# Kernel optimization log

Hardware: AMD Instinct MI355X
Metric: run time of the kernel (lower is better)

## Reference

```python
import jax, jax.numpy as jnp
import numpy as np

B, C, H, W = 16, 256, 32, 32
LN_EPS = 1e-5


def setup_inputs() -> dict:
    key = jax.random.key(0)
    ks = jax.random.split(key, 12)
    s = 1.0 / np.sqrt(C)
    x = jax.random.normal(ks[0], (B, C, H, W), dtype=jnp.float32)
    # Linear weights stored as [in, out] (torch stores [out, in]; math is x @ W_in_out + b)
    wq = jax.random.uniform(ks[1], (C, C), jnp.float32, -s, s)
    bq = jax.random.uniform(ks[2], (C,), jnp.float32, -s, s)
    wk = jax.random.uniform(ks[3], (C, C), jnp.float32, -s, s)
    bk = jax.random.uniform(ks[4], (C,), jnp.float32, -s, s)
    wv = jax.random.uniform(ks[5], (C, C), jnp.float32, -s, s)
    bv = jax.random.uniform(ks[6], (C,), jnp.float32, -s, s)
    w1 = jax.random.uniform(ks[7], (C, C), jnp.float32, -s, s)
    b1 = jax.random.uniform(ks[8], (C,), jnp.float32, -s, s)
    w2 = jax.random.uniform(ks[9], (C, C), jnp.float32, -s, s)
    b2 = jax.random.uniform(ks[10], (C,), jnp.float32, -s, s)
    gamma = jnp.ones((C,), jnp.float32)
    beta = jnp.zeros((C,), jnp.float32)
    return {"x": x, "wq": wq, "bq": bq, "wk": wk, "bk": bk, "wv": wv, "bv": bv,
            "w1": w1, "b1": b1, "w2": w2, "b2": b2, "gamma": gamma, "beta": beta}


def reference(x, wq, bq, wk, bk, wv, bv, w1, b1, w2, b2, gamma, beta):
    Bd, Cd, Hd, Wd = x.shape
    t = x.reshape(Bd, Cd, Hd * Wd).transpose(0, 2, 1)  # [B, N, C]
    q = t @ wq + bq
    k = t @ wk + bk
    v = t @ wv + bv
    # matrix[b,i,j] = q[b,i,:] . k[b,j,:]  (no 1/sqrt(d) scaling, as in source)
    m = jnp.einsum('bic,bjc->bij', q, k)
    # softmax over dim=-2 (the query axis i)
    m = jax.nn.softmax(m, axis=-2)
    # att[b,j,c] = sum_i v[b,i,c] * m[b,i,j]  (v^T @ m, then permute)
    att = jnp.einsum('bic,bij->bjc', v, m)  # [B, N, C]
    # MLP (SiLU, hidden = C), dropout p=0 -> identity; DropPath eval -> identity
    att = jax.nn.silu(att @ w1 + b1) @ w2 + b2
    # LayerNorm over channel dim
    mu = jnp.mean(att, axis=-1, keepdims=True)
    var = jnp.var(att, axis=-1, keepdims=True)
    att = (att - mu) * jax.lax.rsqrt(var + LN_EPS) * gamma + beta
    return att.transpose(0, 2, 1).reshape(Bd, Cd, Hd, Wd)
```

## Files before the change

### kernel.cpp

```cpp
#include <hip/hip_runtime.h>

#define BB 16
#define CC 256
#define NN 1024

typedef _Float16 f16;
typedef __attribute__((ext_vector_type(8))) _Float16 half8;
typedef __attribute__((ext_vector_type(4))) float f32x4;

__device__ __forceinline__ half8 ldg8(const f16* p) {
  return *reinterpret_cast<const half8*>(p);
}

__device__ __forceinline__ void gll16(const f16* g, f16* l) {
  __builtin_amdgcn_global_load_lds((const __attribute__((address_space(1))) void*)g,
                                   (__attribute__((address_space(3))) void*)l, 16, 0, 0);
}

#define VMCNT(n) asm volatile("s_waitcnt vmcnt(" #n ")" ::: "memory")
#define BAR() __builtin_amdgcn_s_barrier()

__device__ __forceinline__ void stage64k(const f16* __restrict__ g, f16* l, int wave, int lane) {
#pragma unroll
  for (int k = 0; k < 16; ++k) {
    int ob = k * 2048 + wave * 512;
    gll16(g + ob + lane * 8, l + ob);
  }
}

struct WP5 {
  const float* s[5];
  f16* d[5];
};

__global__ void __launch_bounds__(256) k_packW(WP5 p) {
  __shared__ float ws[256][17];
  int m = blockIdx.y, ct = blockIdx.x;
  const float* W = p.s[m];
  f16* wp = p.d[m];
  int tid = threadIdx.x;
  int col = tid & 15, cig = tid >> 4;
#pragma unroll
  for (int pg = 0; pg < 16; ++pg) {
    int ci = pg * 16 + cig;
    ws[ci][col] = W[(size_t)ci * 256 + ct * 16 + col];
  }
  __syncthreads();
  int lane = tid & 63, wave = tid >> 6;
  int row16 = lane & 15, quad = lane >> 4;
#pragma unroll
  for (int kk = 0; kk < 2; ++kk) {
    int kc = wave * 2 + kk;
    half8 o;
#pragma unroll
    for (int j = 0; j < 8; ++j) o[j] = (f16)ws[kc * 32 + quad * 8 + j][row16];
    *reinterpret_cast<half8*>(wp + ((size_t)ct * 8 + kc) * 512 + lane * 8) = o;
  }
}

struct QkvSmem {
  union {
    struct { f16 hi[32][264]; f16 lo[32][264]; } ts;
    f16 ex[2][16][264];
    f16 exv[256][40];
  };
};

__global__ void __launch_bounds__(256) k_qkv(const float* __restrict__ x,
    const f16* __restrict__ wqp, const f16* __restrict__ wkp, const f16* __restrict__ wvp,
    const float* __restrict__ bq, const float* __restrict__ bk, const float* __restrict__ bv,
    f16* __restrict__ qp, f16* __restrict__ kp, f16* __restrict__ vp, int b_base) {
  __shared__ QkvSmem sm;
  int bl = blockIdx.x, bg = b_base + bl, n0 = blockIdx.y * 32;
  int tid = threadIdx.x, wave = tid >> 6, lane = tid & 63;
  int row16 = lane & 15, quad = lane >> 4;
  int g = wave >> 1, h = wave & 1;

#pragma unroll
  for (int e = tid; e < 2048; e += 256) {
    int c = e >> 3, n4 = (e & 7) << 2;
    float4 u = *reinterpret_cast<const float4*>(x + (size_t)(bg * CC + c) * NN + n0 + n4);
    float uv[4] = {u.x, u.y, u.z, u.w};
#pragma unroll
    for (int i = 0; i < 4; ++i) {
      f16 hh = (f16)uv[i];
      sm.ts.hi[n4 + i][c] = hh;
      sm.ts.lo[n4 + i][c] = (f16)(uv[i] - (float)hh);
    }
  }
  __syncthreads();

  half8 ah[8], al[8];
#pragma unroll
  for (int kc = 0; kc < 8; ++kc) {
    ah[kc] = *reinterpret_cast<const half8*>(&sm.ts.hi[g * 16 + row16][kc * 32 + quad * 8]);
    al[kc] = *reinterpret_cast<const half8*>(&sm.ts.lo[g * 16 + row16][kc * 32 + quad * 8]);
  }
  __syncthreads();

  const f16* WTs[2]    = {wqp, wkp};
  const float* biases[2] = {bq, bk};
  f16* outs[2]         = {qp, kp};
#pragma unroll
  for (int z = 0; z < 2; ++z) {
    const f16* WT = WTs[z];
    const float* bias = biases[z];
    f16* outp = outs[z];
#pragma unroll
    for (int cp = 0; cp < 2; ++cp) {
      f32x4 acch[4], accl[4];
#pragma unroll
      for (int u = 0; u < 4; ++u) { acch[u] = {0.f,0.f,0.f,0.f}; accl[u] = {0.f,0.f,0.f,0.f}; }
#pragma unroll
      for (int kc = 0; kc < 8; ++kc) {
#pragma unroll
        for (int u = 0; u < 4; ++u) {
          int ct = h * 8 + cp * 4 + u;
          half8 b = ldg8(WT + ((size_t)ct * 8 + kc) * 512 + lane * 8);
          acch[u] = __builtin_amdgcn_mfma_f32_16x16x32_f16(ah[kc], b, acch[u], 0, 0, 0);
          accl[u] = __builtin_amdgcn_mfma_f32_16x16x32_f16(al[kc], b, accl[u], 0, 0, 0);
        }
      }
#pragma unroll
      for (int u = 0; u < 4; ++u) {
        int ct = h * 8 + cp * 4 + u;
        int co = ct * 16 + row16;
        float bb = bias[co];
#pragma unroll
        for (int r = 0; r < 4; ++r)
          sm.ex[g][quad * 4 + r][co] = (f16)(acch[u][r] + accl[u][r] + bb);
      }
    }
    const f16* exr = &sm.ex[g][row16][0];
    size_t fb = ((size_t)bl * 64 + (n0 >> 4) + g) * 8;
#pragma unroll
    for (int k = 0; k < 4; ++k) {
      int kc = h * 4 + k;
      half8 hv = *reinterpret_cast<const half8*>(exr + kc * 32 + quad * 8);
      *reinterpret_cast<half8*>(outp + (fb + kc) * 512 + lane * 8) = hv;
    }
  }
  __syncthreads();

#pragma unroll
  for (int cp = 0; cp < 2; ++cp) {
    f32x4 acch[4], accl[4];
#pragma unroll
    for (int u = 0; u < 4; ++u) { acch[u] = {0.f,0.f,0.f,0.f}; accl[u] = {0.f,0.f,0.f,0.f}; }
#pragma unroll
    for (int kc = 0; kc < 8; ++kc) {
#pragma unroll
      for (int u = 0; u < 4; ++u) {
        int ct = h * 8 + cp * 4 + u;
        half8 b = ldg8(wvp + ((size_t)ct * 8 + kc) * 512 + lane * 8);
        acch[u] = __builtin_amdgcn_mfma_f32_16x16x32_f16(ah[kc], b, acch[u], 0, 0, 0);
        accl[u] = __builtin_amdgcn_mfma_f32_16x16x32_f16(al[kc], b, accl[u], 0, 0, 0);
      }
    }
#pragma unroll
    for (int u = 0; u < 4; ++u) {
      int ct = h * 8 + cp * 4 + u;
      int co = ct * 16 + row16;
      float bb = bv[co];
#pragma unroll
      for (int r = 0; r < 4; ++r)
        sm.exv[co][g * 16 + quad * 4 + r] = (f16)(acch[u][r] + accl[u][r] + bb);
    }
  }
  __syncthreads();
  size_t vb = ((size_t)bl * 32 + blockIdx.y) * 16;
#pragma unroll
  for (int f = 0; f < 4; ++f) {
    int ct = wave * 4 + f;
    half8 o = *reinterpret_cast<const half8*>(&sm.exv[ct * 16 + row16][quad * 8]);
    *reinterpret_cast<half8*>(vp + (vb + ct) * 512 + lane * 8) = o;
  }
}

struct AttnSmem {
  union {
    struct {
      f16 QB[128 * 256];
      f16 VB[128 * 256];
    } s;
    f16 ex[4][16][264];
  } u;
  f16 P[4][4][16][40];
};

__global__ void __launch_bounds__(256) k_attn_mlp(
    const f16* __restrict__ qp, const f16* __restrict__ kp, const f16* __restrict__ vp,
    const f16* __restrict__ w1p, const float* __restrict__ b1,
    const f16* __restrict__ w2p, const float* __restrict__ b2,
    const float* __restrict__ gamma, const float* __restrict__ beta,
    float* __restrict__ out, int b_base) {
  __shared__ AttnSmem sm;
  int bl = blockIdx.x, bg = b_base + bl;
  int j0 = blockIdx.y * 64;
  int tid = threadIdx.x, wave = tid >> 6, lane = tid & 63;
  int row16 = lane & 15, quad = lane >> 4;
  int jw = j0 + wave * 16;

  const f16* kbase = kp + (size_t)bl * NN * CC;
  int jt = (j0 >> 4) + wave;
  half8 kf[8];
#pragma unroll
  for (int kc = 0; kc < 8; ++kc)
    kf[kc] = ldg8(kbase + ((size_t)jt * 8 + kc) * 512 + lane * 8);

  const f16* qbase = qp + (size_t)bl * NN * CC;
  const f16* vbase = vp + (size_t)bl * CC * NN;

  stage64k(qbase, sm.u.s.QB, wave, lane);
  stage64k(vbase, sm.u.s.VB, wave, lane);
  VMCNT(16);
  BAR();

  f32x4 O[16];
#pragma unroll
  for (int ct = 0; ct < 16; ++ct) O[ct] = {0.f, 0.f, 0.f, 0.f};
  float m_run[4], l_lane[4];
#pragma unroll
  for (int r = 0; r < 4; ++r) { m_run[r] = -1e30f; l_lane[r] = 0.f; }

  for (int it = 0; it < 8; ++it) {
    f32x4 s[8];
#pragma unroll
    for (int f = 0; f < 8; ++f) s[f] = {0.f, 0.f, 0.f, 0.f};
#pragma unroll
    for (int kc = 0; kc < 8; ++kc) {
#pragma unroll
      for (int f = 0; f < 8; ++f) {
        half8 b = *reinterpret_cast<const half8*>(&sm.u.s.QB[(f * 8 + kc) * 512 + lane * 8]);
        s[f] = __builtin_amdgcn_mfma_f32_16x16x32_f16(kf[kc], b, s[f], 0, 0, 0);
      }
    }
    BAR();
    stage64k(qbase + (size_t)((it + 1) & 7) * 32768, sm.u.s.QB, wave, lane);

    float alpha[4];
#pragma unroll
    for (int r = 0; r < 4; ++r) {
      float mx = s[0][r];
#pragma unroll
      for (int f = 1; f < 8; ++f) mx = fmaxf(mx, s[f][r]);
#pragma unroll
      for (int off = 1; off < 16; off <<= 1) mx = fmaxf(mx, __shfl_xor(mx, off, 64));
      float mnew = fmaxf(m_run[r], mx);
      alpha[r] = __expf(m_run[r] - mnew);
      m_run[r] = mnew;
      float ps = 0.f;
#pragma unroll
      for (int f = 0; f < 8; ++f) {
        float pv = __expf(s[f][r] - mnew);
        ps += pv;
        sm.P[wave][f >> 1][quad * 4 + r][(f & 1) * 16 + row16] = (f16)pv;
      }
      l_lane[r] = l_lane[r] * alpha[r] + ps;
    }
#pragma unroll
    for (int ct = 0; ct < 16; ++ct)
#pragma unroll
      for (int r = 0; r < 4; ++r) O[ct][r] *= alpha[r];

    VMCNT(16);
    BAR();

#pragma unroll
    for (int c4 = 0; c4 < 4; ++c4) {
      half8 pf = *reinterpret_cast<const half8*>(&sm.P[wave][c4][row16][quad * 8]);
#pragma unroll
      for (int ct = 0; ct < 16; ++ct) {
        half8 vf = *reinterpret_cast<const half8*>(&sm.u.s.VB[(c4 * 16 + ct) * 512 + lane * 8]);
        O[ct] = __builtin_amdgcn_mfma_f32_16x16x32_f16(pf, vf, O[ct], 0, 0, 0);
      }
    }
    BAR();
    stage64k(vbase + (size_t)((it + 1) & 7) * 32768, sm.u.s.VB, wave, lane);
    VMCNT(16);
    BAR();
  }
  VMCNT(0);
  BAR();

  float inv[4];
#pragma unroll
  for (int r = 0; r < 4; ++r) {
    float l = l_lane[r];
#pragma unroll
    for (int off = 1; off < 16; off <<= 1) l += __shfl_xor(l, off, 64);
    inv[r] = 1.f / l;
  }

#pragma unroll
  for (int ct = 0; ct < 16; ++ct)
#pragma unroll
    for (int r = 0; r < 4; ++r)
      sm.u.ex[wave][quad * 4 + r][ct * 16 + row16] = (f16)(O[ct][r] * inv[r]);

  half8 af[8];
#pragma unroll
  for (int kc = 0; kc < 8; ++kc)
    af[kc] = *reinterpret_cast<const half8*>(&sm.u.ex[wave][row16][kc * 32 + quad * 8]);

#pragma unroll
  for (int ct = 0; ct < 16; ++ct) {
    f32x4 acc = {0.f, 0.f, 0.f, 0.f};
    const f16* brow = w1p + ((size_t)ct * 8) * 512 + lane * 8;
#pragma unroll
    for (int kc = 0; kc < 8; ++kc)
      acc = __builtin_amdgcn_mfma_f32_16x16x32_f16(af[kc], ldg8(brow + kc * 512), acc, 0, 0, 0);
    int co = ct * 16 + row16;
    float bb = b1[co];
#pragma unroll
    for (int r = 0; r < 4; ++r) {
      float xg = acc[r] + bb;
      float hh = xg / (1.f + __expf(-xg));
      sm.u.ex[wave][quad * 4 + r][co] = (f16)hh;
    }
  }

  half8 hf[8];
#pragma unroll
  for (int kc = 0; kc < 8; ++kc)
    hf[kc] = *reinterpret_cast<const half8*>(&sm.u.ex[wave][row16][kc * 32 + quad * 8]);

  f32x4 acc2[16];
#pragma unroll
  for (int ct = 0; ct < 16; ++ct) {
    f32x4 acc = {0.f, 0.f, 0.f, 0.f};
    const f16* brow = w2p + ((size_t)ct * 8) * 512 + lane * 8;
#pragma unroll
    for (int kc = 0; kc < 8; ++kc)
      acc = __builtin_amdgcn_mfma_f32_16x16x32_f16(hf[kc], ldg8(brow + kc * 512), acc, 0, 0, 0);
    float bb = b2[ct * 16 + row16];
#pragma unroll
    for (int r = 0; r < 4; ++r) acc[r] += bb;
    acc2[ct] = acc;
  }

  float sum[4] = {0.f, 0.f, 0.f, 0.f}, ssq[4] = {0.f, 0.f, 0.f, 0.f};
#pragma unroll
  for (int ct = 0; ct < 16; ++ct)
#pragma unroll
    for (int r = 0; r < 4; ++r) { float xv = acc2[ct][r]; sum[r] += xv; ssq[r] += xv * xv; }
  float mean[4], rstd[4];
#pragma unroll
  for (int r = 0; r < 4; ++r) {
#pragma unroll
    for (int off = 1; off < 16; off <<= 1) {
      sum[r] += __shfl_xor(sum[r], off, 64);
      ssq[r] += __shfl_xor(ssq[r], off, 64);
    }
    mean[r] = sum[r] * (1.f / 256.f);
    float var = ssq[r] * (1.f / 256.f) - mean[r] * mean[r];
    rstd[r] = rsqrtf(var + 1e-5f);
  }

#pragma unroll
  for (int ct = 0; ct < 16; ++ct) {
    int col = ct * 16 + row16;
    float g = gamma[col], be = beta[col];
    f32x4 v;
#pragma unroll
    for (int r = 0; r < 4; ++r) v[r] = (acc2[ct][r] - mean[r]) * rstd[r] * g + be;
    *reinterpret_cast<f32x4*>(out + (size_t)(bg * CC + col) * NN + jw + quad * 4) = v;
  }
}

extern "C" void kernel_launch(void* const* d_in, const int* in_sizes, int n_in,
                              void* d_out, int out_size, void* d_ws, size_t ws_size,
                              hipStream_t stream) {
  (void)in_sizes; (void)n_in; (void)out_size;
  const float* x     = (const float*)d_in[0];
  const float* wq    = (const float*)d_in[1];
  const float* bq    = (const float*)d_in[2];
  const float* wk    = (const float*)d_in[3];
  const float* bk    = (const float*)d_in[4];
  const float* wv    = (const float*)d_in[5];
  const float* bv    = (const float*)d_in[6];
  const float* w1    = (const float*)d_in[7];
  const float* b1    = (const float*)d_in[8];
  const float* w2    = (const float*)d_in[9];
  const float* b2    = (const float*)d_in[10];
  const float* gamma = (const float*)d_in[11];
  const float* beta  = (const float*)d_in[12];
  float* out = (float*)d_out;

  const size_t WE = 65536;
  const size_t SB = (size_t)NN * CC;
  f16* base = (f16*)d_ws;
  f16* wqp = base + 0 * WE;
  f16* wkp = base + 1 * WE;
  f16* wvp = base + 2 * WE;
  f16* w1p = base + 3 * WE;
  f16* w2p = base + 4 * WE;

  size_t wbytes = 5 * WE * sizeof(f16);
  size_t perb   = 3 * SB * sizeof(f16);
  int nb = (ws_size > wbytes) ? (int)((ws_size - wbytes) / perb) : 1;
  if (nb < 1) nb = 1;
  if (nb > BB) nb = BB;

  f16* qb  = base + 5 * WE;
  f16* kb  = qb + (size_t)nb * SB;
  f16* vTb = kb + (size_t)nb * SB;

  WP5 p;
  p.s[0] = wq; p.s[1] = wk; p.s[2] = wv; p.s[3] = w1; p.s[4] = w2;
  p.d[0] = wqp; p.d[1] = wkp; p.d[2] = wvp; p.d[3] = w1p; p.d[4] = w2p;
  k_packW<<<dim3(16, 5), 256, 0, stream>>>(p);

  for (int b0 = 0; b0 < BB; b0 += nb) {
    int cb = (b0 + nb <= BB) ? nb : (BB - b0);
    k_qkv<<<dim3(cb, 32), 256, 0, stream>>>(x, wqp, wkp, wvp, bq, bk, bv, qb, kb, vTb, b0);
    k_attn_mlp<<<dim3(cb, 16), 256, 0, stream>>>(qb, kb, vTb, w1p, b1, w2p, b2,
                                                 gamma, beta, out, b0);
  }
}
```

Before: 199.6 us.

## Split attention key range across two wave groups with flash-style merge

Doubles the attention+MLP block to 512 threads. Each query tile is now handled by two wave groups that each cover half of every 128-wide key/value chunk, and their partial softmax states (max, sum, O) are merged through shared memory. The MLP output columns and the LayerNorm partial sums are also split between the pair, and output stores become nontemporal. The aim is more waves per block to hide latency and fewer accumulators per wave, at the cost of extra barriers and shared-memory merge traffic.

```diff
diff --git a/kernel.cpp b/kernel.cpp
--- a/kernel.cpp
+++ b/kernel.cpp
@@ -24,6 +24,14 @@
 #pragma unroll
   for (int k = 0; k < 16; ++k) {
     int ob = k * 2048 + wave * 512;
+    gll16(g + ob + lane * 8, l + ob);
+  }
+}
+
+__device__ __forceinline__ void stage64k8(const f16* __restrict__ g, f16* l, int wave, int lane) {
+#pragma unroll
+  for (int k = 0; k < 8; ++k) {
+    int ob = k * 4096 + wave * 512;
     gll16(g + ob + lane * 8, l + ob);
   }
 }
@@ -180,15 +188,23 @@
 struct AttnSmem {
   union {
     struct {
-      f16 QB[128 * 256];
-      f16 VB[128 * 256];
+      f16 QB[2][64 * 256];
+      f16 VB[2][64 * 256];
     } s;
-    f16 ex[4][16][264];
+    struct {
+      union {
+        float Ocmb[4][16][260];
+        f16 ex2[4][16][264];
+      } a;
+      f16 ex[4][16][264];
+    } e;
   } u;
-  f16 P[4][4][16][40];
+  f16 P[8][2][16][40];
+  float ml[8][2][16];
+  float lnbuf[8][2][16];
 };
 
-__global__ void __launch_bounds__(256) k_attn_mlp(
+__global__ void __launch_bounds__(512, 2) k_attn_mlp(
     const f16* __restrict__ qp, const f16* __restrict__ kp, const f16* __restrict__ vp,
     const f16* __restrict__ w1p, const float* __restrict__ b1,
     const f16* __restrict__ w2p, const float* __restrict__ b2,
@@ -199,10 +215,11 @@
   int j0 = blockIdx.y * 64;
   int tid = threadIdx.x, wave = tid >> 6, lane = tid & 63;
   int row16 = lane & 15, quad = lane >> 4;
-  int jw = j0 + wave * 16;
+  int jt_l = wave & 3, p = wave >> 2;
+  int jw = j0 + jt_l * 16;
 
   const f16* kbase = kp + (size_t)bl * NN * CC;
-  int jt = (j0 >> 4) + wave;
+  int jt = (j0 >> 4) + jt_l;
   half8 kf[8];
 #pragma unroll
   for (int kc = 0; kc < 8; ++kc)
@@ -211,9 +228,9 @@
   const f16* qbase = qp + (size_t)bl * NN * CC;
   const f16* vbase = vp + (size_t)bl * CC * NN;
 
-  stage64k(qbase, sm.u.s.QB, wave, lane);
-  stage64k(vbase, sm.u.s.VB, wave, lane);
-  VMCNT(16);
+  stage64k8(qbase, &sm.u.s.QB[0][0], wave, lane);
+  stage64k8(vbase, &sm.u.s.VB[0][0], wave, lane);
+  VMCNT(8);
   BAR();
 
   f32x4 O[16];
@@ -223,27 +240,30 @@
 #pragma unroll
   for (int r = 0; r < 4; ++r) { m_run[r] = -1e30f; l_lane[r] = 0.f; }
 
+  const f16* QBp = &sm.u.s.QB[p][0];
+  const f16* VBp = &sm.u.s.VB[p][0];
+
   for (int it = 0; it < 8; ++it) {
-    f32x4 s[8];
-#pragma unroll
-    for (int f = 0; f < 8; ++f) s[f] = {0.f, 0.f, 0.f, 0.f};
+    f32x4 s[4];
+#pragma unroll
+    for (int f = 0; f < 4; ++f) s[f] = {0.f, 0.f, 0.f, 0.f};
 #pragma unroll
     for (int kc = 0; kc < 8; ++kc) {
 #pragma unroll
-      for (int f = 0; f < 8; ++f) {
-        half8 b = *reinterpret_cast<const half8*>(&sm.u.s.QB[(f * 8 + kc) * 512 + lane * 8]);
+      for (int f = 0; f < 4; ++f) {
+        half8 b = *reinterpret_cast<const half8*>(&QBp[(f * 8 + kc) * 512 + lane * 8]);
         s[f] = __builtin_amdgcn_mfma_f32_16x16x32_f16(kf[kc], b, s[f], 0, 0, 0);
       }
     }
     BAR();
-    stage64k(qbase + (size_t)((it + 1) & 7) * 32768, sm.u.s.QB, wave, lane);
+    stage64k8(qbase + (size_t)((it + 1) & 7) * 32768, &sm.u.s.QB[0][0], wave, lane);
 
     float alpha[4];
 #pragma unroll
     for (int r = 0; r < 4; ++r) {
       float mx = s[0][r];
 #pragma unroll
-      for (int f = 1; f < 8; ++f) mx = fmaxf(mx, s[f][r]);
+      for (int f = 1; f < 4; ++f) mx = fmaxf(mx, s[f][r]);
 #pragma unroll
       for (int off = 1; off < 16; off <<= 1) mx = fmaxf(mx, __shfl_xor(mx, off, 64));
       float mnew = fmaxf(m_run[r], mx);
@@ -251,7 +271,7 @@
       m_run[r] = mnew;
       float ps = 0.f;
 #pragma unroll
-      for (int f = 0; f < 8; ++f) {
+      for (int f = 0; f < 4; ++f) {
         float pv = __expf(s[f][r] - mnew);
         ps += pv;
         sm.P[wave][f >> 1][quad * 4 + r][(f & 1) * 16 + row16] = (f16)pv;
@@ -263,48 +283,84 @@
 #pragma unroll
       for (int r = 0; r < 4; ++r) O[ct][r] *= alpha[r];
 
-    VMCNT(16);
+    VMCNT(8);
     BAR();
 
 #pragma unroll
-    for (int c4 = 0; c4 < 4; ++c4) {
+    for (int c4 = 0; c4 < 2; ++c4) {
       half8 pf = *reinterpret_cast<const half8*>(&sm.P[wave][c4][row16][quad * 8]);
 #pragma unroll
       for (int ct = 0; ct < 16; ++ct) {
-        half8 vf = *reinterpret_cast<const half8*>(&sm.u.s.VB[(c4 * 16 + ct) * 512 + lane * 8]);
+        half8 vf = *reinterpret_cast<const half8*>(&VBp[(c4 * 16 + ct) * 512 + lane * 8]);
         O[ct] = __builtin_amdgcn_mfma_f32_16x16x32_f16(pf, vf, O[ct], 0, 0, 0);
       }
     }
     BAR();
-    stage64k(vbase + (size_t)((it + 1) & 7) * 32768, sm.u.s.VB, wave, lane);
-    VMCNT(16);
+    stage64k8(vbase + (size_t)((it + 1) & 7) * 32768, &sm.u.s.VB[0][0], wave, lane);
+    VMCNT(8);
     BAR();
   }
   VMCNT(0);
   BAR();
 
-  float inv[4];
 #pragma unroll
   for (int r = 0; r < 4; ++r) {
-    float l = l_lane[r];
-#pragma unroll
-    for (int off = 1; off < 16; off <<= 1) l += __shfl_xor(l, off, 64);
-    inv[r] = 1.f / l;
-  }
-
+#pragma unroll
+    for (int off = 1; off < 16; off <<= 1) l_lane[r] += __shfl_xor(l_lane[r], off, 64);
+  }
+  if (row16 == 0) {
+#pragma unroll
+    for (int r = 0; r < 4; ++r) {
+      sm.ml[wave][0][quad * 4 + r] = m_run[r];
+      sm.ml[wave][1][quad * 4 + r] = l_lane[r];
+    }
+  }
+  BAR();
+
+  int partner = wave ^ 4;
+  float alphaS[4], invL[4];
+#pragma unroll
+  for (int r = 0; r < 4; ++r) {
+    int j = quad * 4 + r;
+    float ma = m_run[r], mb = sm.ml[partner][0][j];
+    float M = fmaxf(ma, mb);
+    float la = l_lane[r], lb = sm.ml[partner][1][j];
+    float L = la * __expf(ma - M) + lb * __expf(mb - M);
+    alphaS[r] = __expf(ma - M);
+    invL[r] = 1.f / L;
+  }
 #pragma unroll
   for (int ct = 0; ct < 16; ++ct)
 #pragma unroll
-    for (int r = 0; r < 4; ++r)
-      sm.u.ex[wave][quad * 4 + r][ct * 16 + row16] = (f16)(O[ct][r] * inv[r]);
+    for (int r = 0; r < 4; ++r) O[ct][r] *= alphaS[r];
+
+  if (p == 1) {
+#pragma unroll
+    for (int ct = 0; ct < 16; ++ct)
+#pragma unroll
+      for (int r = 0; r < 4; ++r)
+        sm.u.e.a.Ocmb[jt_l][quad * 4 + r][ct * 16 + row16] = O[ct][r];
+  }
+  BAR();
+  if (p == 0) {
+#pragma unroll
+    for (int ct = 0; ct < 16; ++ct)
+#pragma unroll
+      for (int r = 0; r < 4; ++r) {
+        float v = O[ct][r] + sm.u.e.a.Ocmb[jt_l][quad * 4 + r][ct * 16 + row16];
+        sm.u.e.ex[jt_l][quad * 4 + r][ct * 16 + row16] = (f16)(v * invL[r]);
+      }
+  }
+  BAR();
 
   half8 af[8];
 #pragma unroll
   for (int kc = 0; kc < 8; ++kc)
-    af[kc] = *reinterpret_cast<const half8*>(&sm.u.ex[wave][row16][kc * 32 + quad * 8]);
-
-#pragma unroll
-  for (int ct = 0; ct < 16; ++ct) {
+    af[kc] = *reinterpret_cast<const half8*>(&sm.u.e.ex[jt_l][row16][kc * 32 + quad * 8]);
+
+#pragma unroll
+  for (int q8 = 0; q8 < 8; ++q8) {
+    int ct = p * 8 + q8;
     f32x4 acc = {0.f, 0.f, 0.f, 0.f};
     const f16* brow = w1p + ((size_t)ct * 8) * 512 + lane * 8;
 #pragma unroll
@@ -316,18 +372,20 @@
     for (int r = 0; r < 4; ++r) {
       float xg = acc[r] + bb;
       float hh = xg / (1.f + __expf(-xg));
-      sm.u.ex[wave][quad * 4 + r][co] = (f16)hh;
-    }
-  }
+      sm.u.e.a.ex2[jt_l][quad * 4 + r][co] = (f16)hh;
+    }
+  }
+  BAR();
 
   half8 hf[8];
 #pragma unroll
   for (int kc = 0; kc < 8; ++kc)
-    hf[kc] = *reinterpret_cast<const half8*>(&sm.u.ex[wave][row16][kc * 32 + quad * 8]);
-
-  f32x4 acc2[16];
-#pragma unroll
-  for (int ct = 0; ct < 16; ++ct) {
+    hf[kc] = *reinterpret_cast<const half8*>(&sm.u.e.a.ex2[jt_l][row16][kc * 32 + quad * 8]);
+
+  f32x4 acc2[8];
+#pragma unroll
+  for (int q8 = 0; q8 < 8; ++q8) {
+    int ct = p * 8 + q8;
     f32x4 acc = {0.f, 0.f, 0.f, 0.f};
     const f16* brow = w2p + ((size_t)ct * 8) * 512 + lane * 8;
 #pragma unroll
@@ -336,15 +394,14 @@
     float bb = b2[ct * 16 + row16];
 #pragma unroll
     for (int r = 0; r < 4; ++r) acc[r] += bb;
-    acc2[ct] = acc;
+    acc2[q8] = acc;
   }
 
   float sum[4] = {0.f, 0.f, 0.f, 0.f}, ssq[4] = {0.f, 0.f, 0.f, 0.f};
 #pragma unroll
-  for (int ct = 0; ct < 16; ++ct)
-#pragma unroll
-    for (int r = 0; r < 4; ++r) { float xv = acc2[ct][r]; sum[r] += xv; ssq[r] += xv * xv; }
-  float mean[4], rstd[4];
+  for (int q8 = 0; q8 < 8; ++q8)
+#pragma unroll
+    for (int r = 0; r < 4; ++r) { float xv = acc2[q8][r]; sum[r] += xv; ssq[r] += xv * xv; }
 #pragma unroll
   for (int r = 0; r < 4; ++r) {
 #pragma unroll
@@ -352,19 +409,36 @@
       sum[r] += __shfl_xor(sum[r], off, 64);
       ssq[r] += __shfl_xor(ssq[r], off, 64);
     }
-    mean[r] = sum[r] * (1.f / 256.f);
-    float var = ssq[r] * (1.f / 256.f) - mean[r] * mean[r];
+  }
+  if (row16 == 0) {
+#pragma unroll
+    for (int r = 0; r < 4; ++r) {
+      sm.lnbuf[wave][0][quad * 4 + r] = sum[r];
+      sm.lnbuf[wave][1][quad * 4 + r] = ssq[r];
+    }
+  }
+  BAR();
+
+  float mean[4], rstd[4];
+#pragma unroll
+  for (int r = 0; r < 4; ++r) {
+    int j = quad * 4 + r;
+    float s = sm.lnbuf[wave][0][j] + sm.lnbuf[partner][0][j];
+    float sq = sm.lnbuf[wave][1][j] + sm.lnbuf[partner][1][j];
+    mean[r] = s * (1.f / 256.f);
+    float var = sq * (1.f / 256.f) - mean[r] * mean[r];
     rstd[r] = rsqrtf(var + 1e-5f);
   }
 
 #pragma unroll
-  for (int ct = 0; ct < 16; ++ct) {
-    int col = ct * 16 + row16;
+  for (int q8 = 0; q8 < 8; ++q8) {
+    int col = (p * 8 + q8) * 16 + row16;
     float g = gamma[col], be = beta[col];
     f32x4 v;
 #pragma unroll
-    for (int r = 0; r < 4; ++r) v[r] = (acc2[ct][r] - mean[r]) * rstd[r] * g + be;
-    *reinterpret_cast<f32x4*>(out + (size_t)(bg * CC + col) * NN + jw + quad * 4) = v;
+    for (int r = 0; r < 4; ++r) v[r] = (acc2[q8][r] - mean[r]) * rstd[r] * g + be;
+    __builtin_nontemporal_store(v,
+        reinterpret_cast<f32x4*>(out + (size_t)(bg * CC + col) * NN + jw + quad * 4));
   }
 }
 
@@ -414,7 +488,7 @@
   for (int b0 = 0; b0 < BB; b0 += nb) {
     int cb = (b0 + nb <= BB) ? nb : (BB - b0);
     k_qkv<<<dim3(cb, 32), 256, 0, stream>>>(x, wqp, wkp, wvp, bq, bk, bv, qb, kb, vTb, b0);
-    k_attn_mlp<<<dim3(cb, 16), 256, 0, stream>>>(qb, kb, vTb, w1p, b1, w2p, b2,
+    k_attn_mlp<<<dim3(cb, 16), 512, 0, stream>>>(qb, kb, vTb, w1p, b1, w2p, b2,
                                                  gamma, beta, out, b0);
   }
 }
```

Result: faster. 176.6 us (-11.5%).
